# Performance work log

Hardware: AMD Instinct MI355X
Metric: run time of the kernel (lower is better)

Reference implementation:

```python
import jax, jax.numpy as jnp
import numpy as np

N = 50_000      # node_num
E = 1_600_000   # n_edges (avg degree 32)
D = 256         # input feature dim
H = 128         # GCN / hidden units
FC = 1024       # fc0 units
C = 16          # num_classes


def _tn(key, shape, std=0.1):
    # truncated normal in [-2, 2] std, matching tf.random.truncated_normal(stddev=0.1)
    return jax.random.truncated_normal(key, -2.0, 2.0, shape, jnp.float32) * std


def setup_inputs() -> dict:
    key = jax.random.key(0)
    ks = jax.random.split(key, 16)
    return {
        "x": jax.random.normal(ks[0], (N, D), jnp.float32),
        "edge_index": jax.random.randint(ks[1], (2, E), 0, N, jnp.int32),
        # GCN layer params (tfg GCN: kernel + bias)
        "gcn0_W": _tn(ks[2], (D, H)), "gcn0_b": jnp.zeros((H,), jnp.float32),
        "gcn1_W": _tn(ks[3], (H, H)), "gcn1_b": jnp.zeros((H,), jnp.float32),
        "gcn2_W": _tn(ks[4], (H, H)), "gcn2_b": jnp.zeros((H,), jnp.float32),
        # extra dense block between gcn10 and gcn11
        "w1": _tn(ks[5], (H, H)), "b1": _tn(ks[6], (N, H)),
        # fc head
        "fc0_W": _tn(ks[7], (H, FC)), "fc0_b": jnp.zeros((FC,), jnp.float32),
        "fc1_W": _tn(ks[8], (FC, C)), "fc1_b": jnp.zeros((C,), jnp.float32),
    }


def reference(x, edge_index, gcn0_W, gcn0_b, gcn1_W, gcn1_b, gcn2_W, gcn2_b,
              w1, b1, fc0_W, fc0_b, fc1_W, fc1_b):
    n = x.shape[0]
    src, dst = edge_index[0], edge_index[1]
    loops = jnp.arange(n, dtype=src.dtype)
    # GCN renormalization trick: A_hat = A + I, w_ij = deg_i^-1/2 * deg_j^-1/2
    src_f = jnp.concatenate([src, loops])   # [E+N]
    dst_f = jnp.concatenate([dst, loops])
    deg = jax.ops.segment_sum(jnp.ones(src_f.shape[0], jnp.float32), src_f, num_segments=n)
    norm = jnp.where(deg > 0, deg, 1.0) ** -0.5
    ew = norm[src_f] * norm[dst_f]          # [E+N]

    def gcn(h, W, b):
        h = h @ W                                                      # [N,H]
        agg = jax.ops.segment_sum(h[src_f] * ew[:, None], dst_f, num_segments=n)
        return agg + b

    h1 = jax.nn.relu(gcn(x, gcn0_W, gcn0_b))       # gcn10, relu
    h11 = jax.nn.relu(h1 @ w1 + b1)                # dense with per-node bias
    h2 = gcn(h11, gcn1_W, gcn1_b)                  # gcn11, no activation
    h2 = jax.nn.relu(gcn(h2, gcn2_W, gcn2_b))      # gcn12, relu
    h = h1 + h2
    h = jax.nn.relu(h @ fc0_W + fc0_b)             # fc0
    return h @ fc1_W + fc1_b                       # fc1 logits [N,C]
```

## Files before the change

kernel.cpp:

```cpp
#include <hip/hip_runtime.h>
#include <hip/hip_bf16.h>
#include <hip/hip_fp16.h>
#include <cstddef>
#include <cstdint>

#define NNODES 50000
#define NEDGES 1600000
#define DIM 256
#define HID 128
#define FCU 1024
#define NCLS 16

#define NBKT 256
#define BW 196
#define NBLK_A 64
#define EPB (NEDGES / NBLK_A)
#define CAPB 8192

#define DCHUNK 12800
#define DSLICE 64
#define DEPB (NEDGES / DSLICE)

typedef short s16x8 __attribute__((ext_vector_type(8)));
typedef _Float16 f16x8 __attribute__((ext_vector_type(8)));
typedef float f32x4 __attribute__((ext_vector_type(4)));
#define MFMA16 __builtin_amdgcn_mfma_f32_16x16x32_bf16
#define MFMAH  __builtin_amdgcn_mfma_f32_16x16x32_f16

typedef unsigned short u16;
typedef unsigned int u32;

__device__ inline u16 f2bf(float f) {
    u32 u = __float_as_uint(f);
    return (u16)((u + 0x7FFF + ((u >> 16) & 1)) >> 16);
}
__device__ inline float bf2f(u16 h) { return __uint_as_float(((u32)h) << 16); }
__device__ inline void split2(float v, u16& h, u16& l) {
    h = f2bf(v);
    l = f2bf(v - bf2f(h));
}


__global__ __launch_bounds__(256) void histDeg(const int* __restrict__ ei, int* __restrict__ degS) {
    __shared__ int h[DCHUNK];
    int chunk = blockIdx.x >> 6;
    int slice = blockIdx.x & (DSLICE - 1);
    int t = threadIdx.x;
    int base0 = chunk * DCHUNK;
    for (int i = t; i < DCHUNK; i += 256) h[i] = 0;
    __syncthreads();
    int base = slice * DEPB;
    for (int e = base + t; e < base + DEPB; e += 256) {
        int s = ei[e] - base0;
        if ((unsigned)s < (unsigned)DCHUNK) atomicAdd(&h[s], 1);
    }
    __syncthreads();
    int lim = NNODES - base0; if (lim > DCHUNK) lim = DCHUNK;
    for (int i = t; i < lim; i += 256) {
        int v = h[i];
        if (v) atomicAdd(&degS[base0 + i], v);
    }
}

__global__ void norm_kernel(const int* __restrict__ degS, float* __restrict__ nrm) {
    int i = blockIdx.x * blockDim.x + threadIdx.x;
    if (i < NNODES) nrm[i] = rsqrtf((float)(degS[i] + 1));
}

__global__ __launch_bounds__(1024) void histA(const int* __restrict__ ei, int* __restrict__ hist) {
    __shared__ int h[NBKT];
    int blk = blockIdx.x, t = threadIdx.x;
    if (t < NBKT) h[t] = 0;
    __syncthreads();
    int base = blk * EPB;
    for (int e = base + t; e < base + EPB; e += 1024) {
        int dst = ei[NEDGES + e];
        atomicAdd(&h[dst / BW], 1);
    }
    __syncthreads();
    if (t < NBKT) hist[t * NBLK_A + blk] = h[t];
}

__global__ __launch_bounds__(1024) void scanh_a(int* __restrict__ hist, int* __restrict__ bsum) {
    __shared__ int s[1024];
    int b = blockIdx.x, t = threadIdx.x, i = b * 1024 + t;
    int v = hist[i];
    s[t] = v;
    __syncthreads();
    for (int off = 1; off < 1024; off <<= 1) {
        int x = (t >= off) ? s[t - off] : 0;
        __syncthreads();
        s[t] += x;
        __syncthreads();
    }
    hist[i] = s[t] - v;
    if (t == 1023) bsum[b] = s[1023];
}
__global__ void scanh_b(int* __restrict__ bsum) {
    if (threadIdx.x == 0 && blockIdx.x == 0) {
        int a = 0;
        for (int j = 0; j < 16; ++j) { int t = bsum[j]; bsum[j] = a; a += t; }
    }
}
__global__ __launch_bounds__(1024) void scanh_c(int* __restrict__ hist, const int* __restrict__ bsum) {
    int i = blockIdx.x * 1024 + threadIdx.x;
    hist[i] += bsum[blockIdx.x];
}

__global__ __launch_bounds__(1024) void bucket_fill(const int* __restrict__ ei,
                                                    const int* __restrict__ hist,
                                                    u32* __restrict__ packed) {
    __shared__ int cur[NBKT];
    int blk = blockIdx.x, t = threadIdx.x;
    if (t < NBKT) cur[t] = hist[t * NBLK_A + blk];
    __syncthreads();
    int base = blk * EPB;
    for (int e = base + t; e < base + EPB; e += 1024) {
        int src = ei[e], dst = ei[NEDGES + e];
        int p = atomicAdd(&cur[dst / BW], 1);
        packed[p] = ((u32)dst << 16) | (u32)src;
    }
}

__global__ __launch_bounds__(256) void bucket_csr(const u32* __restrict__ packed,
                                                  const int* __restrict__ hist,
                                                  int* __restrict__ rowptr, u16* __restrict__ csr) {
    __shared__ u32 st[CAPB];
    __shared__ u16 so[CAPB];
    __shared__ int cnt[256], excl[256];
    int b = blockIdx.x, t = threadIdx.x;
    int ebase = hist[b * NBLK_A];
    int eend  = (b < NBKT - 1) ? hist[(b + 1) * NBLK_A] : NEDGES;
    int nE = eend - ebase;
    if (nE > CAPB) nE = CAPB;
    cnt[t] = 0;
    __syncthreads();
    for (int i = t; i < nE; i += 256) {
        u32 p = packed[ebase + i];
        st[i] = p;
        atomicAdd(&cnt[(int)(p >> 16) - b * BW], 1);
    }
    __syncthreads();
    int v = cnt[t];
    excl[t] = v;
    __syncthreads();
    for (int off = 1; off < 256; off <<= 1) {
        int x = (t >= off) ? excl[t - off] : 0;
        __syncthreads();
        excl[t] += x;
        __syncthreads();
    }
    int ex = excl[t] - v;
    int node = b * BW + t;
    if (t < BW && node < NNODES) rowptr[node] = ebase + ex;
    if (b == NBKT - 1 && t == 0) rowptr[NNODES] = NEDGES;
    cnt[t] = ex;
    __syncthreads();
    for (int i = t; i < nE; i += 256) {
        u32 p = st[i];
        int pos = atomicAdd(&cnt[(int)(p >> 16) - b * BW], 1);
        so[pos] = (u16)(p & 0xFFFF);
    }
    __syncthreads();
    for (int i = t; i < nE; i += 256) csr[ebase + i] = so[i];
}


__global__ __launch_bounds__(256) void conv_x(const float* __restrict__ x,
                                              u16* __restrict__ xh, u16* __restrict__ xl) {
    int i = blockIdx.x * blockDim.x + threadIdx.x;
    const float4 v = *reinterpret_cast<const float4*>(x + (size_t)i * 4);
    u16 h0, l0, h1, l1, h2, l2, h3, l3;
    split2(v.x, h0, l0); split2(v.y, h1, l1); split2(v.z, h2, l2); split2(v.w, h3, l3);
    ushort4 hv = make_ushort4(h0, h1, h2, h3), lv = make_ushort4(l0, l1, l2, l3);
    *reinterpret_cast<ushort4*>(xh + (size_t)i * 4) = hv;
    *reinterpret_cast<ushort4*>(xl + (size_t)i * 4) = lv;
}

__global__ __launch_bounds__(256) void conv_wT(const float* __restrict__ W, int K, int N,
                                               u16* __restrict__ outH, u16* __restrict__ outL) {
    int o = blockIdx.x * blockDim.x + threadIdx.x;
    if (o < K * N) {
        int n = o / K, k = o - n * K;
        u16 h, l;
        split2(W[(size_t)k * N + n], h, l);
        outH[o] = h; outL[o] = l;
    }
}

__global__ __launch_bounds__(256) void conv_weights(
    const float* __restrict__ fc0W, u16* __restrict__ F0Th,
    const float* __restrict__ w1,    u16* __restrict__ w1Th,
    const float* __restrict__ gcn1W, u16* __restrict__ W1Th,
    const float* __restrict__ gcn2W, u16* __restrict__ W2Th,
    const float* __restrict__ fc1W,  __half* __restrict__ W1f)
{
    int b = blockIdx.x, t = threadIdx.x;
    if (b < 512) {
        int o = b * 256 + t;
        int n = o >> 7, k = o & 127;
        F0Th[o] = f2bf(fc0W[(size_t)k * FCU + n]);
    } else if (b < 576) {
        int o = (b - 512) * 256 + t;
        int n = o >> 7, k = o & 127;
        w1Th[o] = f2bf(w1[(size_t)k * HID + n]);
    } else if (b < 640) {
        int o = (b - 576) * 256 + t;
        int n = o >> 7, k = o & 127;
        W1Th[o] = f2bf(gcn1W[(size_t)k * HID + n]);
    } else if (b < 704) {
        int o = (b - 640) * 256 + t;
        int n = o >> 7, k = o & 127;
        W2Th[o] = f2bf(gcn2W[(size_t)k * HID + n]);
    } else {
        int o = (b - 704) * 256 + t;
        int n = o >> 10, k = o & 1023;
        W1f[o] = __float2half(fc1W[(size_t)k * NCLS + n]);
    }
}


template<int VAR, int WLO>
__global__ __launch_bounds__(256) void agg_fast(
    const __half* __restrict__ g, const float* __restrict__ nrm,
    const int* __restrict__ rowptr, const u16* __restrict__ csr,
    const float* __restrict__ bias,
    u16* __restrict__ outH, u16* __restrict__ outL)
{
    int w = threadIdx.x >> 6, lane = threadIdx.x & 63;
    int i = blockIdx.x * 4 + w;
    if (i >= NNODES) return;
    const __half2* gp = reinterpret_cast<const __half2*>(g);
    size_t lrow = (size_t)i * 64 + lane;
    float2 acc = __half22float2(gp[lrow]);
    int e0 = rowptr[i], e1 = rowptr[i + 1];
    int e = e0;
    for (; e + 8 <= e1; e += 8) {
        int s[8];
#pragma unroll
        for (int q = 0; q < 8; ++q) s[q] = csr[e + q];
        __half2 v[8];
#pragma unroll
        for (int q = 0; q < 8; ++q) v[q] = gp[(size_t)s[q] * 64 + lane];
#pragma unroll
        for (int q = 0; q < 8; ++q) {
            float2 f = __half22float2(v[q]);
            acc.x += f.x; acc.y += f.y;
        }
    }
    for (; e < e1; ++e) {
        int s = csr[e];
        float2 f = __half22float2(gp[(size_t)s * 64 + lane]);
        acc.x += f.x; acc.y += f.y;
    }
    float ni = nrm[i];
    const float2 b = *reinterpret_cast<const float2*>(bias + lane * 2);
    float v0 = fmaf(ni, acc.x, b.x);
    float v1 = fmaf(ni, acc.y, b.y);
    if (VAR != 1) { v0 = fmaxf(v0, 0.f); v1 = fmaxf(v1, 0.f); }
    if (WLO) {
        u16 h0, l0, h1v, l1v;
        split2(v0, h0, l0);
        split2(v1, h1v, l1v);
        *reinterpret_cast<ushort2*>(outH + (size_t)i * HID + lane * 2) = make_ushort2(h0, h1v);
        *reinterpret_cast<ushort2*>(outL + (size_t)i * HID + lane * 2) = make_ushort2(l0, l1v);
    } else {
        *reinterpret_cast<ushort2*>(outH + (size_t)i * HID + lane * 2) = make_ushort2(f2bf(v0), f2bf(v1));
    }
}


template<int K, int MODE, int PL>
__global__ __launch_bounds__(256) void gemm_split(
    const u16* __restrict__ Ah, const u16* __restrict__ Al,
    const u16* __restrict__ BTh, const u16* __restrict__ BTl,
    const float* __restrict__ pnb, const float* __restrict__ nrmv,
    __half* __restrict__ outG, u16* __restrict__ outH, int M)
{
    const int PK = 40;
    __shared__ __align__(16) u16 AsH[64 * PK];
    __shared__ __align__(16) u16 BsH[128 * PK];
    __shared__ __align__(16) u16 AsL[PL == 3 ? 64 * PK : 1];
    __shared__ __align__(16) u16 BsL[PL == 3 ? 128 * PK : 1];
    int tid = threadIdx.x, lane = tid & 63, w = tid >> 6;
    int wr = w >> 1, wc = w & 1;
    int l15 = lane & 15, l4 = lane >> 4;
    int blockRow = blockIdx.x * 64;
    f32x4 acc[2][4] = {};

    for (int kk = 0; kk < K; kk += 32) {
        {
            int row = tid >> 2, kc = (tid & 3) * 8;
            int gr = blockRow + row; if (gr >= M) gr = M - 1;
            *(s16x8*)&AsH[row * PK + kc] = *(const s16x8*)&Ah[(size_t)gr * K + kk + kc];
            if (PL == 3)
                *(s16x8*)&AsL[row * PK + kc] = *(const s16x8*)&Al[(size_t)gr * K + kk + kc];
        }
#pragma unroll
        for (int i2 = 0; i2 < 2; ++i2) {
            int idx = tid + i2 * 256;
            int n = idx >> 2, kc = (idx & 3) * 8;
            *(s16x8*)&BsH[n * PK + kc] = *(const s16x8*)&BTh[(size_t)n * K + kk + kc];
            if (PL == 3)
                *(s16x8*)&BsL[n * PK + kc] = *(const s16x8*)&BTl[(size_t)n * K + kk + kc];
        }
        __syncthreads();
        s16x8 ah[2], al[2], bh[4], bl[4];
#pragma unroll
        for (int mi = 0; mi < 2; ++mi) {
            ah[mi] = *(const s16x8*)&AsH[(wr * 32 + mi * 16 + l15) * PK + 8 * l4];
            if (PL == 3) al[mi] = *(const s16x8*)&AsL[(wr * 32 + mi * 16 + l15) * PK + 8 * l4];
        }
#pragma unroll
        for (int ni = 0; ni < 4; ++ni) {
            bh[ni] = *(const s16x8*)&BsH[(wc * 64 + ni * 16 + l15) * PK + 8 * l4];
            if (PL == 3) bl[ni] = *(const s16x8*)&BsL[(wc * 64 + ni * 16 + l15) * PK + 8 * l4];
        }
#pragma unroll
        for (int mi = 0; mi < 2; ++mi)
#pragma unroll
            for (int ni = 0; ni < 4; ++ni) {
                acc[mi][ni] = MFMA16(ah[mi], bh[ni], acc[mi][ni], 0, 0, 0);
                if (PL == 3) {
                    acc[mi][ni] = MFMA16(ah[mi], bl[ni], acc[mi][ni], 0, 0, 0);
                    acc[mi][ni] = MFMA16(al[mi], bh[ni], acc[mi][ni], 0, 0, 0);
                }
            }
        __syncthreads();
    }
#pragma unroll
    for (int mi = 0; mi < 2; ++mi)
#pragma unroll
        for (int ni = 0; ni < 4; ++ni) {
            int c = wc * 64 + ni * 16 + l15;
#pragma unroll
            for (int j = 0; j < 4; ++j) {
                int r = blockRow + wr * 32 + mi * 16 + l4 * 4 + j;
                if (r < M) {
                    if (MODE == 0) {
                        outG[(size_t)r * 128 + c] = __float2half(nrmv[r] * acc[mi][ni][j]);
                    } else {
                        float v = fmaxf(acc[mi][ni][j] + pnb[(size_t)r * 128 + c], 0.f);
                        outH[(size_t)r * 128 + c] = f2bf(v);
                    }
                }
            }
        }
}


__global__ __launch_bounds__(256) void agg_fc(
    const __half* __restrict__ g, const float* __restrict__ nrm,
    const int* __restrict__ rowptr, const u16* __restrict__ csr,
    const float* __restrict__ bias,
    const u16* __restrict__ h1H, const u16* __restrict__ h1L,
    const u16* __restrict__ BTh,
    const float* __restrict__ fc0b,
    const __half* __restrict__ W1f,
    const float* __restrict__ fc1b,
    float* __restrict__ out, int M)
{
    __shared__ __align__(16) u16 hA[32 * 128];
    __shared__ __align__(16) u16 vs[32 * 128];
    __shared__ __align__(16) u16 W1s[16 * 128];
    int tid = threadIdx.x, lane = tid & 63, w = tid >> 6;
    int l15 = lane & 15, l4 = lane >> 4;
    int blockRow = blockIdx.x * 32;

    s16x8 bcur[2][4];
#pragma unroll
    for (int ni = 0; ni < 2; ++ni)
#pragma unroll
        for (int ks = 0; ks < 4; ++ks)
            bcur[ni][ks] = *(const s16x8*)&BTh[(size_t)(w * 32 + ni * 16 + l15) * HID + ks * 32 + 8 * l4];

    const __half2* gp = reinterpret_cast<const __half2*>(g);
    const float2 bb = *reinterpret_cast<const float2*>(bias + lane * 2);
    int colc = lane >> 2;
    int colr = (lane * 2) & 7;
#pragma unroll 1
    for (int k = 0; k < 8; ++k) {
        int row = w * 8 + k;
        int i = blockRow + row;
        float v0 = 0.f, v1 = 0.f;
        if (i < M) {
            float2 acc = __half22float2(gp[(size_t)i * 64 + lane]);
            int e0 = rowptr[i], e1 = rowptr[i + 1];
            int e = e0;
            for (; e + 8 <= e1; e += 8) {
                int s[8];
#pragma unroll
                for (int q = 0; q < 8; ++q) s[q] = csr[e + q];
                __half2 vv[8];
#pragma unroll
                for (int q = 0; q < 8; ++q) vv[q] = gp[(size_t)s[q] * 64 + lane];
#pragma unroll
                for (int q = 0; q < 8; ++q) {
                    float2 f = __half22float2(vv[q]);
                    acc.x += f.x; acc.y += f.y;
                }
            }
            for (; e < e1; ++e) {
                float2 f = __half22float2(gp[(size_t)csr[e] * 64 + lane]);
                acc.x += f.x; acc.y += f.y;
            }
            float ni_ = nrm[i];
            v0 = fmaxf(fmaf(ni_, acc.x, bb.x), 0.f);
            v1 = fmaxf(fmaf(ni_, acc.y, bb.y), 0.f);
            ushort2 rh = *reinterpret_cast<const ushort2*>(h1H + (size_t)i * HID + lane * 2);
            ushort2 rl = *reinterpret_cast<const ushort2*>(h1L + (size_t)i * HID + lane * 2);
            v0 += bf2f(rh.x) + bf2f(rl.x);
            v1 += bf2f(rh.y) + bf2f(rl.y);
        }
        int cs = colc ^ (row & 7);
        *reinterpret_cast<ushort2*>(&hA[row * 128 + (cs << 3) + colr]) =
            make_ushort2(f2bf(v0), f2bf(v1));
    }
    __syncthreads();

    s16x8 ahr[2][4];
#pragma unroll
    for (int mi = 0; mi < 2; ++mi) {
        int row = mi * 16 + l15;
#pragma unroll
        for (int ks = 0; ks < 4; ++ks)
            ahr[mi][ks] = *(const s16x8*)&hA[row * 128 + (((ks * 4 + l4) ^ (row & 7)) << 3)];
    }

    f32x4 acc2 = {0.f, 0.f, 0.f, 0.f};
#pragma unroll
    for (int cc = 0; cc < FCU / 128; ++cc) {
        int co = cc * 128;
        s16x8 bnxt[2][4];
        if (cc + 1 < FCU / 128) {
#pragma unroll
            for (int ni = 0; ni < 2; ++ni)
#pragma unroll
                for (int ks = 0; ks < 4; ++ks)
                    bnxt[ni][ks] = *(const s16x8*)&BTh[(size_t)(co + 128 + w * 32 + ni * 16 + l15) * HID + ks * 32 + 8 * l4];
        }

        f32x4 acc[2][2] = {};
#pragma unroll
        for (int ks = 0; ks < 4; ++ks)
#pragma unroll
            for (int mi = 0; mi < 2; ++mi)
#pragma unroll
                for (int ni = 0; ni < 2; ++ni)
                    acc[mi][ni] = MFMA16(ahr[mi][ks], bcur[ni][ks], acc[mi][ni], 0, 0, 0);

        {
            int cls = tid >> 4, kc = (tid & 15) * 8;
            s16x8 t = *(const s16x8*)&W1f[(size_t)cls * FCU + co + kc];
            *(s16x8*)&W1s[cls * 128 + (kc ^ ((cls & 7) << 3))] = t;
        }
#pragma unroll
        for (int mi = 0; mi < 2; ++mi)
#pragma unroll
            for (int ni = 0; ni < 2; ++ni) {
                int unit = w * 32 + ni * 16 + l15;
                float b0v = fc0b[co + unit];
#pragma unroll
                for (int j = 0; j < 4; ++j) {
                    int rl = mi * 16 + l4 * 4 + j;
                    float v = fmaxf(acc[mi][ni][j] + b0v, 0.f);
                    vs[rl * 128 + (unit ^ ((rl & 7) << 3))] = __half_as_ushort(__float2half(v));
                }
            }
        __syncthreads();

        if (w < 2) {
#pragma unroll
            for (int ks = 0; ks < 4; ++ks) {
                int row = w * 16 + l15;
                int colk = ks * 32 + 8 * l4;
                f16x8 a2 = *(const f16x8*)&vs[row * 128 + (colk ^ ((row & 7) << 3))];
                f16x8 b2 = *(const f16x8*)&W1s[l15 * 128 + (colk ^ ((l15 & 7) << 3))];
                acc2 = MFMAH(a2, b2, acc2, 0, 0, 0);
            }
        }
        __syncthreads();

        if (cc + 1 < FCU / 128) {
#pragma unroll
            for (int ni = 0; ni < 2; ++ni)
#pragma unroll
                for (int ks = 0; ks < 4; ++ks)
                    bcur[ni][ks] = bnxt[ni][ks];
        }
    }

    if (w < 2) {
#pragma unroll
        for (int j = 0; j < 4; ++j) {
            int gr = blockRow + w * 16 + l4 * 4 + j;
            if (gr < M) out[(size_t)gr * NCLS + l15] = acc2[j] + fc1b[l15];
        }
    }
}


extern "C" void kernel_launch(void* const* d_in, const int* in_sizes, int n_in,
                              void* d_out, int out_size, void* d_ws, size_t ws_size,
                              hipStream_t stream)
{
    const float* x     = (const float*)d_in[0];
    const int*   ei    = (const int*)d_in[1];
    const float* gcn0W = (const float*)d_in[2];
    const float* gcn0b = (const float*)d_in[3];
    const float* gcn1W = (const float*)d_in[4];
    const float* gcn1b = (const float*)d_in[5];
    const float* gcn2W = (const float*)d_in[6];
    const float* gcn2b = (const float*)d_in[7];
    const float* w1    = (const float*)d_in[8];
    const float* b1    = (const float*)d_in[9];
    const float* fc0W  = (const float*)d_in[10];
    const float* fc0b  = (const float*)d_in[11];
    const float* fc1W  = (const float*)d_in[12];
    const float* fc1b  = (const float*)d_in[13];
    float* out = (float*)d_out;

    char* ws = (char*)d_ws;
    size_t off = 0;
    auto alloc = [&](size_t bytes) -> void* {
        void* p = ws + off;
        off = (off + bytes + 255) & ~(size_t)255;
        return p;
    };
    int* degS   = (int*)alloc((size_t)NNODES * 4);
    int* rowptr = (int*)alloc((size_t)(NNODES + 1) * 4);
    int* hist   = (int*)alloc((size_t)NBKT * NBLK_A * 4);
    int* bsum   = (int*)alloc(64 * 4);
    u32* packed = (u32*)alloc((size_t)NEDGES * 4);
    u16* csr    = (u16*)alloc((size_t)NEDGES * 2);
    float* nrm  = (float*)alloc((size_t)NNODES * 4);
    u16* W0Th = (u16*)alloc((size_t)DIM * HID * 2);  u16* W0Tl = (u16*)alloc((size_t)DIM * HID * 2);
    u16* w1Th = (u16*)alloc((size_t)HID * HID * 2);
    u16* W1Th = (u16*)alloc((size_t)HID * HID * 2);
    u16* W2Th = (u16*)alloc((size_t)HID * HID * 2);
    u16* F0Th = (u16*)alloc((size_t)HID * FCU * 2);
    __half* W1f = (__half*)alloc((size_t)FCU * NCLS * 2);
    __half* bufG = (__half*)alloc((size_t)NNODES * HID * 2);
    u16* R1 = (u16*)alloc((size_t)2 * NNODES * DIM * 2);
    u16* xh = R1, *xl = R1 + (size_t)NNODES * DIM;
    u16* h1H = R1,                            *h1L = R1 + (size_t)NNODES * HID;
    u16* B3H = R1 + (size_t)2 * NNODES * HID;

    const int M = NNODES;
    hipMemsetAsync(degS, 0, (size_t)NNODES * 4, stream);

    histDeg<<<4 * DSLICE, 256, 0, stream>>>(ei, degS);
    norm_kernel<<<(NNODES + 255) / 256, 256, 0, stream>>>(degS, nrm);
    histA<<<NBLK_A, 1024, 0, stream>>>(ei, hist);
    scanh_a<<<16, 1024, 0, stream>>>(hist, bsum);
    scanh_b<<<1, 64, 0, stream>>>(bsum);
    scanh_c<<<16, 1024, 0, stream>>>(hist, bsum);
    bucket_fill<<<NBLK_A, 1024, 0, stream>>>(ei, hist, packed);
    bucket_csr<<<NBKT, 256, 0, stream>>>(packed, hist, rowptr, csr);

    conv_x<<<(NNODES * DIM / 4 + 255) / 256, 256, 0, stream>>>(x, xh, xl);
    conv_wT<<<(DIM * HID + 255) / 256, 256, 0, stream>>>(gcn0W, DIM, HID, W0Th, W0Tl);
    conv_weights<<<768, 256, 0, stream>>>(fc0W, F0Th, w1, w1Th, gcn1W, W1Th, gcn2W, W2Th, fc1W, W1f);

    const int GB = (M + 63) / 64;
    const int GB32 = (M + 31) / 32;
    const int AB = (NNODES + 3) / 4;
    gemm_split<DIM, 0, 3><<<GB, 256, 0, stream>>>(xh, xl, W0Th, W0Tl, nullptr, nrm, bufG, nullptr, M);
    agg_fast<0, 1><<<AB, 256, 0, stream>>>(bufG, nrm, rowptr, csr, gcn0b, h1H, h1L);
    gemm_split<HID, 2, 1><<<GB, 256, 0, stream>>>(h1H, nullptr, w1Th, nullptr, b1, nullptr, nullptr, B3H, M);
    gemm_split<HID, 0, 1><<<GB, 256, 0, stream>>>(B3H, nullptr, W1Th, nullptr, nullptr, nrm, bufG, nullptr, M);
    agg_fast<1, 0><<<AB, 256, 0, stream>>>(bufG, nrm, rowptr, csr, gcn1b, B3H, nullptr);
    gemm_split<HID, 0, 1><<<GB, 256, 0, stream>>>(B3H, nullptr, W2Th, nullptr, nullptr, nrm, bufG, nullptr, M);
    agg_fc<<<GB32, 256, 0, stream>>>(bufG, nrm, rowptr, csr, gcn2b, h1H, h1L,
                                     F0Th, fc0b, W1f, fc1b, out, M);
}
```

Measured before the change: 470.7 us.

## Split fused final aggregation+FC kernel into separate aggregation and FC kernels

Unfuses the last GCN aggregation from the FC head. A new agg_fast variant adds the h1 residual and writes bf16 h to a buffer, and a separate fc_kernel then reads it. This gives the aggregation one wave per node with 4 nodes per block, instead of a serial 8-row loop per wave inside the GEMM block, which should improve latency hiding for the gather. The cost is an extra kernel launch and an extra round trip of the N×128 bf16 activations through global memory.

```diff
diff --git a/kernel.cpp b/kernel.cpp
--- a/kernel.cpp
+++ b/kernel.cpp
@@ -225,6 +225,7 @@
     const __half* __restrict__ g, const float* __restrict__ nrm,
     const int* __restrict__ rowptr, const u16* __restrict__ csr,
     const float* __restrict__ bias,
+    const u16* __restrict__ h1H, const u16* __restrict__ h1L,
     u16* __restrict__ outH, u16* __restrict__ outL)
 {
     int w = threadIdx.x >> 6, lane = threadIdx.x & 63;
@@ -258,6 +259,12 @@
     float v0 = fmaf(ni, acc.x, b.x);
     float v1 = fmaf(ni, acc.y, b.y);
     if (VAR != 1) { v0 = fmaxf(v0, 0.f); v1 = fmaxf(v1, 0.f); }
+    if (VAR == 2) {
+        ushort2 rh = *reinterpret_cast<const ushort2*>(h1H + (size_t)i * HID + lane * 2);
+        ushort2 rl = *reinterpret_cast<const ushort2*>(h1L + (size_t)i * HID + lane * 2);
+        v0 += bf2f(rh.x) + bf2f(rl.x);
+        v1 += bf2f(rh.y) + bf2f(rl.y);
+    }
     if (WLO) {
         u16 h0, l0, h1v, l1v;
         split2(v0, h0, l0);
@@ -349,24 +356,30 @@
 }
 
 
-__global__ __launch_bounds__(256) void agg_fc(
-    const __half* __restrict__ g, const float* __restrict__ nrm,
-    const int* __restrict__ rowptr, const u16* __restrict__ csr,
-    const float* __restrict__ bias,
-    const u16* __restrict__ h1H, const u16* __restrict__ h1L,
+__global__ __launch_bounds__(256) void fc_kernel(
+    const u16* __restrict__ Ahi,
     const u16* __restrict__ BTh,
     const float* __restrict__ fc0b,
     const __half* __restrict__ W1f,
     const float* __restrict__ fc1b,
     float* __restrict__ out, int M)
 {
-    __shared__ __align__(16) u16 hA[32 * 128];
     __shared__ __align__(16) u16 vs[32 * 128];
     __shared__ __align__(16) u16 W1s[16 * 128];
     int tid = threadIdx.x, lane = tid & 63, w = tid >> 6;
     int l15 = lane & 15, l4 = lane >> 4;
     int blockRow = blockIdx.x * 32;
 
+    s16x8 ahr[2][4];
+#pragma unroll
+    for (int mi = 0; mi < 2; ++mi) {
+        int r = blockRow + mi * 16 + l15; if (r >= M) r = M - 1;
+#pragma unroll
+        for (int ks = 0; ks < 4; ++ks)
+            ahr[mi][ks] = *(const s16x8*)&Ahi[(size_t)r * HID + ks * 32 + 8 * l4];
+    }
+
+    f32x4 acc2 = {0.f, 0.f, 0.f, 0.f};
     s16x8 bcur[2][4];
 #pragma unroll
     for (int ni = 0; ni < 2; ++ni)
@@ -374,60 +387,6 @@
         for (int ks = 0; ks < 4; ++ks)
             bcur[ni][ks] = *(const s16x8*)&BTh[(size_t)(w * 32 + ni * 16 + l15) * HID + ks * 32 + 8 * l4];
 
-    const __half2* gp = reinterpret_cast<const __half2*>(g);
-    const float2 bb = *reinterpret_cast<const float2*>(bias + lane * 2);
-    int colc = lane >> 2;
-    int colr = (lane * 2) & 7;
-#pragma unroll 1
-    for (int k = 0; k < 8; ++k) {
-        int row = w * 8 + k;
-        int i = blockRow + row;
-        float v0 = 0.f, v1 = 0.f;
-        if (i < M) {
-            float2 acc = __half22float2(gp[(size_t)i * 64 + lane]);
-            int e0 = rowptr[i], e1 = rowptr[i + 1];
-            int e = e0;
-            for (; e + 8 <= e1; e += 8) {
-                int s[8];
-#pragma unroll
-                for (int q = 0; q < 8; ++q) s[q] = csr[e + q];
-                __half2 vv[8];
-#pragma unroll
-                for (int q = 0; q < 8; ++q) vv[q] = gp[(size_t)s[q] * 64 + lane];
-#pragma unroll
-                for (int q = 0; q < 8; ++q) {
-                    float2 f = __half22float2(vv[q]);
-                    acc.x += f.x; acc.y += f.y;
-                }
-            }
-            for (; e < e1; ++e) {
-                float2 f = __half22float2(gp[(size_t)csr[e] * 64 + lane]);
-                acc.x += f.x; acc.y += f.y;
-            }
-            float ni_ = nrm[i];
-            v0 = fmaxf(fmaf(ni_, acc.x, bb.x), 0.f);
-            v1 = fmaxf(fmaf(ni_, acc.y, bb.y), 0.f);
-            ushort2 rh = *reinterpret_cast<const ushort2*>(h1H + (size_t)i * HID + lane * 2);
-            ushort2 rl = *reinterpret_cast<const ushort2*>(h1L + (size_t)i * HID + lane * 2);
-            v0 += bf2f(rh.x) + bf2f(rl.x);
-            v1 += bf2f(rh.y) + bf2f(rl.y);
-        }
-        int cs = colc ^ (row & 7);
-        *reinterpret_cast<ushort2*>(&hA[row * 128 + (cs << 3) + colr]) =
-            make_ushort2(f2bf(v0), f2bf(v1));
-    }
-    __syncthreads();
-
-    s16x8 ahr[2][4];
-#pragma unroll
-    for (int mi = 0; mi < 2; ++mi) {
-        int row = mi * 16 + l15;
-#pragma unroll
-        for (int ks = 0; ks < 4; ++ks)
-            ahr[mi][ks] = *(const s16x8*)&hA[row * 128 + (((ks * 4 + l4) ^ (row & 7)) << 3)];
-    }
-
-    f32x4 acc2 = {0.f, 0.f, 0.f, 0.f};
 #pragma unroll
     for (int cc = 0; cc < FCU / 128; ++cc) {
         int co = cc * 128;
@@ -566,11 +525,11 @@
     const int GB32 = (M + 31) / 32;
     const int AB = (NNODES + 3) / 4;
     gemm_split<DIM, 0, 3><<<GB, 256, 0, stream>>>(xh, xl, W0Th, W0Tl, nullptr, nrm, bufG, nullptr, M);
-    agg_fast<0, 1><<<AB, 256, 0, stream>>>(bufG, nrm, rowptr, csr, gcn0b, h1H, h1L);
+    agg_fast<0, 1><<<AB, 256, 0, stream>>>(bufG, nrm, rowptr, csr, gcn0b, nullptr, nullptr, h1H, h1L);
     gemm_split<HID, 2, 1><<<GB, 256, 0, stream>>>(h1H, nullptr, w1Th, nullptr, b1, nullptr, nullptr, B3H, M);
     gemm_split<HID, 0, 1><<<GB, 256, 0, stream>>>(B3H, nullptr, W1Th, nullptr, nullptr, nrm, bufG, nullptr, M);
-    agg_fast<1, 0><<<AB, 256, 0, stream>>>(bufG, nrm, rowptr, csr, gcn1b, B3H, nullptr);
+    agg_fast<1, 0><<<AB, 256, 0, stream>>>(bufG, nrm, rowptr, csr, gcn1b, nullptr, nullptr, B3H, nullptr);
     gemm_split<HID, 0, 1><<<GB, 256, 0, stream>>>(B3H, nullptr, W2Th, nullptr, nullptr, nrm, bufG, nullptr, M);
-    agg_fc<<<GB32, 256, 0, stream>>>(bufG, nrm, rowptr, csr, gcn2b, h1H, h1L,
-                                     F0Th, fc0b, W1f, fc1b, out, M);
-}
+    agg_fast<2, 0><<<AB, 256, 0, stream>>>(bufG, nrm, rowptr, csr, gcn2b, h1H, h1L, B3H, nullptr);
+    fc_kernel<<<GB32, 256, 0, stream>>>(B3H, F0Th, fc0b, W1f, fc1b, out, M);
+}
```

Result: faster. 412.4 us (-12.4%).
